# Kernel tuning notes

Hardware: AMD Instinct MI355X
Metric: run time of the kernel (lower is better)

Reference implementation:

```python
import jax, jax.numpy as jnp
import numpy as np

N = 1_000_000   # users
M = 500_000     # items
K = 64          # latent dim
GAMMA = (1.0, 1.0, 1.0, 1.0)
N_BASKET = 64


def setup_inputs() -> dict:
    key = jax.random.key(0)
    k1, k2, k3, k4, k5, k6 = jax.random.split(key, 6)
    P = N + 2 * M
    # sparse one-hot/multi-hot transaction vector
    x = jnp.zeros((P,), dtype=jnp.float32)
    u_idx = 12345          # user one-hot
    t_idx = 678            # target-item one-hot
    rng = np.random.default_rng(0)
    b_idx = rng.choice(M, size=N_BASKET, replace=False)  # basket multi-hot
    x = x.at[u_idx].set(1.0).at[N + t_idx].set(1.0)
    x = x.at[N + M + jnp.asarray(b_idx)].set(1.0)
    delta = jnp.ones((1,), dtype=jnp.float32)  # label in {+1,-1}
    pmi = jnp.zeros((1,), dtype=jnp.float32)   # unused by forward
    # learned parameters
    w_0 = jax.random.normal(k1, (1,), dtype=jnp.float32)
    w_bias = jax.random.uniform(k2, (P, 1), dtype=jnp.float32)
    u_V = jax.random.normal(k3, (N, K), dtype=jnp.float32)
    t_V = jax.random.normal(k4, (M, K), dtype=jnp.float32)
    b_V = jax.random.normal(k5, (M, K), dtype=jnp.float32)
    return {"x": x, "delta": delta, "pmi": pmi, "w_0": w_0,
            "w_bias": w_bias, "u_V": u_V, "t_V": t_V, "b_V": b_V}


def _fm(t, w_0, w_bias, u_V, t_V, b_V):
    # t: (n+2m,) one-hot/multi-hot transaction
    bias = jnp.dot(t, w_bias[:, 0])                 # scalar
    u_vec = t[:N] @ u_V                             # (k,)
    t_vec = t[N:N + M] @ t_V                        # (k,)
    xb = t[N + M:N + 2 * M]                         # basket mask (m,)
    sum_b = xb @ b_V                                # sum_i b_i     (k,)
    sum_b_sq = xb @ jnp.sum(b_V * b_V, axis=1)      # sum_i ||b_i||^2
    u_t = jnp.dot(u_vec, t_vec)
    t_b = jnp.dot(t_vec, sum_b)                     # sum_i <t, b_i>
    bs = 0.5 * (jnp.dot(sum_b, sum_b) - sum_b_sq)   # sum_{i<j} <b_i, b_j>
    u_b = jnp.dot(u_vec, sum_b)                     # sum_i <u, b_i>
    y = (w_0[0] + bias + GAMMA[0] * u_t + GAMMA[1] * t_b
         + GAMMA[2] * bs + GAMMA[3] * u_b)
    return y.reshape(1, 1)                          # match torch (1,1)


def reference(x, delta, pmi, w_0, w_bias, u_V, t_V, b_V):
    t = x[:N + 2 * M]
    y = _fm(t, w_0, w_bias, u_V, t_V, b_V)
    return jax.nn.sigmoid(y * delta[0])
```

## Files before the change

kernel.cpp:

```cpp
#include <hip/hip_runtime.h>
#include <math.h>

#define N_U 1000000
#define M_T 500000
#define P_TOT (N_U + 2 * M_T)
#define KDIM 64

#define WS_BIAS 0
#define WS_SBSQ 1
#define WS_U 8
#define WS_T 72
#define WS_B 136
#define WS_FLOATS 256

__global__ void zero_ws_kernel(float* __restrict__ ws) {
    int i = threadIdx.x;
    if (i < WS_FLOATS) ws[i] = 0.0f;
}

__global__ void scan_accum_kernel(const float* __restrict__ x,
                                  const float* __restrict__ w_bias,
                                  const float* __restrict__ u_V,
                                  const float* __restrict__ t_V,
                                  const float* __restrict__ b_V,
                                  float* __restrict__ ws,
                                  int P) {
    int gid = blockIdx.x * blockDim.x + threadIdx.x;
    long long base = (long long)gid * 4;
    if (base >= P) return;

    float4 v = *reinterpret_cast<const float4*>(x + base);
    float vals[4] = {v.x, v.y, v.z, v.w};

#pragma unroll
    for (int j = 0; j < 4; ++j) {
        long long i = base + j;
        if (i >= P) break;
        float xv = vals[j];
        if (xv != 0.0f) {
            atomicAdd(&ws[WS_BIAS], xv * w_bias[i]);
            const float* row;
            float* acc;
            bool is_b = false;
            if (i < N_U) {
                row = u_V + i * KDIM;
                acc = ws + WS_U;
            } else if (i < (long long)N_U + M_T) {
                row = t_V + (i - N_U) * KDIM;
                acc = ws + WS_T;
            } else {
                row = b_V + (i - N_U - M_T) * KDIM;
                acc = ws + WS_B;
                is_b = true;
            }
            float nrm = 0.0f;
#pragma unroll
            for (int k = 0; k < KDIM; ++k) {
                float rv = row[k];
                atomicAdd(&acc[k], xv * rv);
                nrm += rv * rv;
            }
            if (is_b) atomicAdd(&ws[WS_SBSQ], xv * nrm);
        }
    }
}

__global__ void finalize_kernel(const float* __restrict__ ws,
                                const float* __restrict__ w0,
                                const float* __restrict__ delta,
                                float* __restrict__ out) {
    int k = threadIdx.x;
    float u = ws[WS_U + k];
    float t = ws[WS_T + k];
    float b = ws[WS_B + k];

    float ut = u * t;
    float tb = t * b;
    float bb = b * b;
    float ub = u * b;

#pragma unroll
    for (int off = 32; off > 0; off >>= 1) {
        ut += __shfl_down(ut, off);
        tb += __shfl_down(tb, off);
        bb += __shfl_down(bb, off);
        ub += __shfl_down(ub, off);
    }

    if (k == 0) {
        float bias = ws[WS_BIAS];
        float sbsq = ws[WS_SBSQ];
        float bs = 0.5f * (bb - sbsq);
        float y = w0[0] + bias + ut + tb + bs + ub;
        float z = y * delta[0];
        out[0] = 1.0f / (1.0f + expf(-z));
    }
}

extern "C" void kernel_launch(void* const* d_in, const int* in_sizes, int n_in,
                              void* d_out, int out_size, void* d_ws, size_t ws_size,
                              hipStream_t stream) {
    const float* x      = (const float*)d_in[0];
    const float* delta  = (const float*)d_in[1];
    const float* w0     = (const float*)d_in[3];
    const float* w_bias = (const float*)d_in[4];
    const float* u_V    = (const float*)d_in[5];
    const float* t_V    = (const float*)d_in[6];
    const float* b_V    = (const float*)d_in[7];
    float* out = (float*)d_out;
    float* ws  = (float*)d_ws;

    int P = in_sizes[0];

    hipLaunchKernelGGL(zero_ws_kernel, dim3(1), dim3(256), 0, stream, ws);

    int nvec = (P + 3) / 4;
    int blocks = (nvec + 255) / 256;
    hipLaunchKernelGGL(scan_accum_kernel, dim3(blocks), dim3(256), 0, stream,
                       x, w_bias, u_V, t_V, b_V, ws, P);

    hipLaunchKernelGGL(finalize_kernel, dim3(1), dim3(64), 0, stream,
                       ws, w0, delta, out);
}
```

Before: 417.9 us.

## Fuse finalize into scan via last-block reduction with fixed grid-stride launch

Merges the separate finalize kernel into the scan kernel. A completion counter in the workspace lets the last block to finish read the accumulators, using atomic reads for coherence, and compute the sigmoid. The scan now runs a fixed grid of 256 blocks, each thread handling 8 float4 slots strided across the grid, instead of one block per 1024 elements. This removes one kernel launch and most block-scheduling overhead, at the cost of a serialized tail in the last block and fewer resident wavefronts to hide memory latency.

```diff
diff --git a/kernel.cpp b/kernel.cpp
--- a/kernel.cpp
+++ b/kernel.cpp
@@ -3,7 +3,6 @@
 
 #define N_U 1000000
 #define M_T 500000
-#define P_TOT (N_U + 2 * M_T)
 #define KDIM 64
 
 #define WS_BIAS 0
@@ -11,74 +10,97 @@
 #define WS_U 8
 #define WS_T 72
 #define WS_B 136
+#define WS_DONE 248
 #define WS_FLOATS 256
 
-__global__ void zero_ws_kernel(float* __restrict__ ws) {
+#define SCAN_BLOCKS 256
+#define SCAN_THREADS 256
+#define VEC_PER_THREAD 8
+
+__global__ void init_ws_kernel(float* __restrict__ ws) {
     int i = threadIdx.x;
     if (i < WS_FLOATS) ws[i] = 0.0f;
 }
 
-__global__ void scan_accum_kernel(const float* __restrict__ x,
-                                  const float* __restrict__ w_bias,
-                                  const float* __restrict__ u_V,
-                                  const float* __restrict__ t_V,
-                                  const float* __restrict__ b_V,
-                                  float* __restrict__ ws,
-                                  int P) {
-    int gid = blockIdx.x * blockDim.x + threadIdx.x;
-    long long base = (long long)gid * 4;
-    if (base >= P) return;
+__device__ __forceinline__ float coherent_read(float* p) {
+    return atomicAdd(p, 0.0f);
+}
 
-    float4 v = *reinterpret_cast<const float4*>(x + base);
-    float vals[4] = {v.x, v.y, v.z, v.w};
+__global__ void __launch_bounds__(SCAN_THREADS)
+scan_finalize_kernel(const float* __restrict__ x,
+                     const float* __restrict__ w_bias,
+                     const float* __restrict__ u_V,
+                     const float* __restrict__ t_V,
+                     const float* __restrict__ b_V,
+                     const float* __restrict__ w0,
+                     const float* __restrict__ delta,
+                     float* __restrict__ ws,
+                     float* __restrict__ out,
+                     int P) {
+    const int gid = blockIdx.x * blockDim.x + threadIdx.x;
+    const int nthreads = SCAN_BLOCKS * SCAN_THREADS;
+    const int nvec = (P + 3) / 4;
 
 #pragma unroll
-    for (int j = 0; j < 4; ++j) {
-        long long i = base + j;
-        if (i >= P) break;
-        float xv = vals[j];
-        if (xv != 0.0f) {
-            atomicAdd(&ws[WS_BIAS], xv * w_bias[i]);
-            const float* row;
-            float* acc;
-            bool is_b = false;
-            if (i < N_U) {
-                row = u_V + i * KDIM;
-                acc = ws + WS_U;
-            } else if (i < (long long)N_U + M_T) {
-                row = t_V + (i - N_U) * KDIM;
-                acc = ws + WS_T;
-            } else {
-                row = b_V + (i - N_U - M_T) * KDIM;
-                acc = ws + WS_B;
-                is_b = true;
+    for (int it = 0; it < VEC_PER_THREAD; ++it) {
+        int slot = gid + it * nthreads;
+        if (slot >= nvec) break;
+        long long base = (long long)slot * 4;
+        float4 v = *reinterpret_cast<const float4*>(x + base);
+        float vals[4] = {v.x, v.y, v.z, v.w};
+#pragma unroll
+        for (int j = 0; j < 4; ++j) {
+            long long i = base + j;
+            if (i >= P) break;
+            float xv = vals[j];
+            if (xv != 0.0f) {
+                atomicAdd(&ws[WS_BIAS], xv * w_bias[i]);
+                const float* row;
+                float* acc;
+                bool is_b = false;
+                if (i < N_U) {
+                    row = u_V + i * KDIM;
+                    acc = ws + WS_U;
+                } else if (i < (long long)N_U + M_T) {
+                    row = t_V + (i - N_U) * KDIM;
+                    acc = ws + WS_T;
+                } else {
+                    row = b_V + (i - N_U - M_T) * KDIM;
+                    acc = ws + WS_B;
+                    is_b = true;
+                }
+                float nrm = 0.0f;
+#pragma unroll
+                for (int k = 0; k < KDIM; ++k) {
+                    float rv = row[k];
+                    atomicAdd(&acc[k], xv * rv);
+                    nrm += rv * rv;
+                }
+                if (is_b) atomicAdd(&ws[WS_SBSQ], xv * nrm);
             }
-            float nrm = 0.0f;
-#pragma unroll
-            for (int k = 0; k < KDIM; ++k) {
-                float rv = row[k];
-                atomicAdd(&acc[k], xv * rv);
-                nrm += rv * rv;
-            }
-            if (is_b) atomicAdd(&ws[WS_SBSQ], xv * nrm);
         }
     }
-}
 
-__global__ void finalize_kernel(const float* __restrict__ ws,
-                                const float* __restrict__ w0,
-                                const float* __restrict__ delta,
-                                float* __restrict__ out) {
+    __shared__ int is_last;
+    __syncthreads();
+    if (threadIdx.x == 0) {
+        __threadfence();
+        int old = atomicAdd((int*)(ws + WS_DONE), 1);
+        is_last = (old == SCAN_BLOCKS - 1) ? 1 : 0;
+    }
+    __syncthreads();
+    if (!is_last || threadIdx.x >= 64) return;
+
+    __threadfence();
     int k = threadIdx.x;
-    float u = ws[WS_U + k];
-    float t = ws[WS_T + k];
-    float b = ws[WS_B + k];
+    float u = coherent_read(ws + WS_U + k);
+    float t = coherent_read(ws + WS_T + k);
+    float b = coherent_read(ws + WS_B + k);
 
     float ut = u * t;
     float tb = t * b;
     float bb = b * b;
     float ub = u * b;
-
 #pragma unroll
     for (int off = 32; off > 0; off >>= 1) {
         ut += __shfl_down(ut, off);
@@ -88,8 +110,8 @@
     }
 
     if (k == 0) {
-        float bias = ws[WS_BIAS];
-        float sbsq = ws[WS_SBSQ];
+        float bias = coherent_read(ws + WS_BIAS);
+        float sbsq = coherent_read(ws + WS_SBSQ);
         float bs = 0.5f * (bb - sbsq);
         float y = w0[0] + bias + ut + tb + bs + ub;
         float z = y * delta[0];
@@ -112,13 +134,7 @@
 
     int P = in_sizes[0];
 
-    hipLaunchKernelGGL(zero_ws_kernel, dim3(1), dim3(256), 0, stream, ws);
-
-    int nvec = (P + 3) / 4;
-    int blocks = (nvec + 255) / 256;
-    hipLaunchKernelGGL(scan_accum_kernel, dim3(blocks), dim3(256), 0, stream,
-                       x, w_bias, u_V, t_V, b_V, ws, P);
-
-    hipLaunchKernelGGL(finalize_kernel, dim3(1), dim3(64), 0, stream,
-                       ws, w0, delta, out);
+    hipLaunchKernelGGL(init_ws_kernel, dim3(1), dim3(256), 0, stream, ws);
+    hipLaunchKernelGGL(scan_finalize_kernel, dim3(SCAN_BLOCKS), dim3(SCAN_THREADS),
+                       0, stream, x, w_bias, u_V, t_V, b_V, w0, delta, ws, out, P);
 }
```

Result: no change. 424.6 us (+1.6%).
